# Kernel tuning notes

Hardware: AMD Instinct MI355X
Metric: run time of the kernel (lower is better)

The kernel has to match this reference:

```python
import jax, jax.numpy as jnp
import numpy as np

EPS = 0.01       # perturbation radius (constructor arg)
MEAN = 0.1307    # MNIST normalize constants from the 'else' branch
SIGMA = 0.3081


def _get_bound(v, eps):
    # torch get_bound detaches eps before taking |.| and summing
    r = jnp.sum(jnp.abs(jax.lax.stop_gradient(eps)), axis=-1)
    return v + r, v - r


def _relu_zono(v, eps):
    # v: [N], eps: [N, E]. Append one fresh (zero) error column, as the torch code does.
    n = v.shape[0]
    eps = jnp.concatenate([eps, jnp.zeros((n, 1), eps.dtype)], axis=-1)  # [N, E+1]
    u, l = _get_bound(v, eps)
    denom = u - l  # = 2*sum|eps| >= 0; guard against 0 for non-crossing rows
    # slopes are created as Parameters = u/(u-l) on the first pass (detached leaf)
    slope = jax.lax.stop_gradient(u / jnp.where(denom == 0, 1.0, denom))
    # at init slope == base = u/(u-l), so the slope <= base branch is taken
    term = (1.0 - slope) * u * 0.5
    crossing = (u > 0) & (l < 0)
    dead = u <= 0
    # torch uses slope.data * values.data for the linear part, + term (term carries grad)
    v_cross = jax.lax.stop_gradient(slope * v) + term
    v_new = jnp.where(dead, 0.0, jnp.where(crossing, v_cross, v))
    eps_cross = jnp.concatenate([slope[:, None] * eps[:, :-1], term[:, None]], axis=-1)
    eps_new = jnp.where(dead[:, None], 0.0, jnp.where(crossing[:, None], eps_cross, eps))
    return v_new, eps_new


def _forward(inputs, W1, b1, W2, b2, W3, b3):
    # initial zonotope build (faithful to source: values = u + l, radii = values - l = u)
    upper = jnp.minimum(inputs + EPS, 1.0)   # upper - relu(upper - 1)
    lower = jnp.maximum(inputs - EPS, 0.0)   # relu(lower)
    values = upper + lower
    eps = jnp.diag((values - lower).flatten())  # [D, D]
    # Normalize layer (the 'else' branch)
    values = (values - MEAN) / SIGMA
    eps = eps / SIGMA
    # Flatten
    v = values.flatten()
    # Linear -> ReLU -> Linear -> ReLU -> Linear
    v = W1 @ v + b1
    eps = W1 @ eps
    v, eps = _relu_zono(v, eps)
    v = W2 @ v + b2
    eps = W2 @ eps
    v, eps = _relu_zono(v, eps)
    v = W3 @ v + b3
    eps = W3 @ eps
    u, l = _get_bound(v, eps)
    return u, l


def setup_inputs() -> dict:
    key = jax.random.key(0)
    ks = jax.random.split(key, 7)
    D, H, O = 1024, 4096, 10
    inputs = jax.random.uniform(ks[0], (1, 1, 32, 32), jnp.float32)
    W1 = jax.random.normal(ks[1], (H, D), jnp.float32) / np.float32(np.sqrt(D))
    b1 = jax.random.normal(ks[2], (H,), jnp.float32) * 0.01
    W2 = jax.random.normal(ks[3], (H, H), jnp.float32) / np.float32(np.sqrt(H))
    b2 = jax.random.normal(ks[4], (H,), jnp.float32) * 0.01
    W3 = jax.random.normal(ks[5], (O, H), jnp.float32) / np.float32(np.sqrt(H))
    b3 = jax.random.normal(ks[6], (O,), jnp.float32) * 0.01
    return {"inputs": inputs, "W1": W1, "b1": b1, "W2": W2, "b2": b2, "W3": W3, "b3": b3}


def reference(inputs, W1, b1, W2, b2, W3, b3):
    return _forward(inputs, W1, b1, W2, b2, W3, b3)
```

## Files before the change

kernel.cpp:

```cpp
#include <hip/hip_runtime.h>
#include <math.h>

#define ZEPS  0.01f
#define ZMEAN 0.1307f
#define ZSIGMA 0.3081f

constexpr int D = 1024, H = 4096, O = 10;

using short8 = __attribute__((ext_vector_type(8))) short;
using f32x4  = __attribute__((ext_vector_type(4))) float;
typedef unsigned short ushort_t;

__device__ inline unsigned short f2bf(float x) {
    unsigned int u = __float_as_uint(x);
    u += 0x7FFFu + ((u >> 16) & 1u);
    return (unsigned short)(u >> 16);
}
__device__ inline float bf2f(unsigned short h) {
    return __uint_as_float(((unsigned int)h) << 16);
}

__device__ inline unsigned int f2bf2_fast(float a, float b) {
    unsigned int ua = __float_as_uint(a) + 0x8000u;
    unsigned int ub = __float_as_uint(b) + 0x8000u;
    return (ua >> 16) | (ub & 0xFFFF0000u);
}

__device__ inline void gl_lds16(const void* g, void* l) {
    __builtin_amdgcn_global_load_lds(
        (const __attribute__((address_space(1))) unsigned int*)g,
        (__attribute__((address_space(3))) unsigned int*)l, 16, 0, 0);
}

__device__ inline float zval(float xv) {
    float up = fminf(xv + ZEPS, 1.f);
    float lo = fmaxf(xv - ZEPS, 0.f);
    return (up + lo - ZMEAN) / ZSIGMA;
}
__device__ inline float zdia(float xv) {
    return fminf(xv + ZEPS, 1.f) / ZSIGMA;
}

__device__ inline void relu_params(float v, float r, float& vout, float& aout, float& tout) {
    float u = v + r, l = v - r;
    float denom = u - l;
    float slope = u / (denom == 0.f ? 1.f : denom);
    float term = (1.f - slope) * u * 0.5f;
    bool dead = (u <= 0.f);
    bool crossing = (u > 0.f) && (l < 0.f);
    vout = dead ? 0.f : (crossing ? (slope * v + term) : v);
    aout = dead ? 0.f : (crossing ? slope : 1.f);
    tout = (!dead && crossing) ? term : 0.f;
}

__global__ __launch_bounds__(256) void k_layer1(const float* __restrict__ W1, const float* __restrict__ b1,
                                                const float* __restrict__ x,
                                                float* __restrict__ v1p, float* __restrict__ a1,
                                                float* __restrict__ t1) {
    int wid = threadIdx.x >> 6, lane = threadIdx.x & 63;
    int i = blockIdx.x * 4 + wid;
    const float* row = W1 + (size_t)i * D;
    float sv = 0.f, sr = 0.f;
#pragma unroll
    for (int it = 0; it < 4; ++it) {
        int j = it * 256 + lane * 4;
        float4 w = *(const float4*)&row[j];
        float4 xx = *(const float4*)&x[j];
        sv += w.x * zval(xx.x) + w.y * zval(xx.y) + w.z * zval(xx.z) + w.w * zval(xx.w);
        sr += fabsf(w.x) * zdia(xx.x) + fabsf(w.y) * zdia(xx.y) +
              fabsf(w.z) * zdia(xx.z) + fabsf(w.w) * zdia(xx.w);
    }
#pragma unroll
    for (int m = 1; m <= 32; m <<= 1) {
        sv += __shfl_xor(sv, m, 64);
        sr += __shfl_xor(sr, m, 64);
    }
    if (lane == 0) {
        float vo, ao, to;
        relu_params(sv + b1[i], sr, vo, ao, to);
        v1p[i] = vo; a1[i] = ao; t1[i] = to;
    }
}

__global__ __launch_bounds__(256) void k_scaleT(const float* __restrict__ W1, const float* __restrict__ a1,
                                                const float* __restrict__ x,
                                                ushort_t* __restrict__ W1sT) {
    __shared__ float tile[32][33];
    int j0 = blockIdx.x * 32, k0 = blockIdx.y * 32;
    int r = threadIdx.x >> 3;
    int c = (threadIdx.x & 7) * 4;
    float4 w = *(const float4*)&W1[(size_t)(k0 + r) * D + j0 + c];
    float4 xx = *(const float4*)&x[j0 + c];
    float a = a1[k0 + r];
    tile[r][c + 0] = a * w.x * zdia(xx.x);
    tile[r][c + 1] = a * w.y * zdia(xx.y);
    tile[r][c + 2] = a * w.z * zdia(xx.z);
    tile[r][c + 3] = a * w.w * zdia(xx.w);
    __syncthreads();
    ushort4 o;
    o.x = f2bf(tile[c + 0][r]);
    o.y = f2bf(tile[c + 1][r]);
    o.z = f2bf(tile[c + 2][r]);
    o.w = f2bf(tile[c + 3][r]);
    *(ushort4*)&W1sT[(size_t)(j0 + r) * H + k0 + c] = o;
}

#define GBK 64
__global__ __launch_bounds__(256) void k_gemm_mfma(const float* __restrict__ A,
                                                   const ushort_t* __restrict__ B,
                                                   const float* __restrict__ v1p,
                                                   const float* __restrict__ t1,
                                                   ushort_t* __restrict__ C,
                                                   float* __restrict__ vpart,
                                                   float* __restrict__ tpart) {
    const int N = D, K = H;
    __shared__ __align__(16) ushort_t As[2][128 * GBK];
    __shared__ __align__(16) ushort_t Bs[2][128 * GBK];
    __shared__ float vt[2048], tt[2048];
    int b = blockIdx.x;
    int u = b & 7, v = b >> 3;
    int z = u >> 2;
    int y = (u & 3) * 8 + (v >> 3);
    int xb = v & 7;
    int tid = threadIdx.x;
    int wave = tid >> 6, lane = tid & 63;
    int bm = y * 128, bn = xb * 128;
    int kbeg = z * (K / 2);
    ushort_t* Cz = C + (size_t)z * ((size_t)H * D);
    int wm = (wave >> 1) * 64, wn = (wave & 1) * 64;

    int srow = lane >> 3, sc = lane & 7, scp = sc ^ srow;
    int r15 = lane & 15, quad = lane >> 4, key = r15 & 7;
    int rowg = tid >> 3, ch = tid & 7;
    int aswz = ch ^ (rowg & 7);

    const int S = (K / 2) / GBK;

    float4 pa[4][2];
    float sv[4] = {0.f, 0.f, 0.f, 0.f}, st[4] = {0.f, 0.f, 0.f, 0.f};

    auto issueA = [&](int s) {
#pragma unroll
        for (int g = 0; g < 4; ++g) {
            const float* ap = &A[(size_t)(bm + g * 32 + rowg) * K + kbeg + s * GBK + ch * 8];
            pa[g][0] = *(const float4*)ap;
            pa[g][1] = *(const float4*)(ap + 4);
        }
    };
    auto issueB = [&](int s, int buf) {
#pragma unroll
        for (int g = 0; g < 2; ++g) {
            int row = wave * 32 + g * 16;
            (void)row;
        }
#pragma unroll
        for (int g = 0; g < 4; ++g) {
            int row = wave * 32 + g * 8;
            gl_lds16(&B[(size_t)(bn + row + srow) * K + kbeg + s * GBK + scp * 8], &Bs[buf][row * GBK]);
        }
    };
    auto cvtwrite = [&](int s, int buf) {
        if ((s & 7) == xb) {
            const float* vp = &vt[s * 64 + ch * 8];
            const float* tp = &tt[s * 64 + ch * 8];
            float4 v0 = *(const float4*)vp, v1 = *(const float4*)(vp + 4);
            float4 t0 = *(const float4*)tp, t1v = *(const float4*)(tp + 4);
#pragma unroll
            for (int g = 0; g < 4; ++g) {
                sv[g] += pa[g][0].x * v0.x + pa[g][0].y * v0.y + pa[g][0].z * v0.z + pa[g][0].w * v0.w
                       + pa[g][1].x * v1.x + pa[g][1].y * v1.y + pa[g][1].z * v1.z + pa[g][1].w * v1.w;
                st[g] += pa[g][0].x * t0.x + pa[g][0].y * t0.y + pa[g][0].z * t0.z + pa[g][0].w * t0.w
                       + pa[g][1].x * t1v.x + pa[g][1].y * t1v.y + pa[g][1].z * t1v.z + pa[g][1].w * t1v.w;
            }
        }
#pragma unroll
        for (int g = 0; g < 4; ++g) {
            uint4 hh;
            hh.x = f2bf2_fast(pa[g][0].x, pa[g][0].y);
            hh.y = f2bf2_fast(pa[g][0].z, pa[g][0].w);
            hh.z = f2bf2_fast(pa[g][1].x, pa[g][1].y);
            hh.w = f2bf2_fast(pa[g][1].z, pa[g][1].w);
            *(uint4*)&As[buf][(g * 32 + rowg) * GBK + aswz * 8] = hh;
        }
    };

    f32x4 acc[4][4];
#pragma unroll
    for (int p = 0; p < 4; ++p)
#pragma unroll
        for (int q = 0; q < 4; ++q) acc[p][q] = (f32x4){0.f, 0.f, 0.f, 0.f};

    issueA(0);
    issueB(0, 0);
    for (int idx = tid; idx < 512; idx += 256) {
        *(float4*)&vt[idx * 4] = *(const float4*)&v1p[kbeg + idx * 4];
        *(float4*)&tt[idx * 4] = *(const float4*)&t1[kbeg + idx * 4];
    }
    __syncthreads();
    cvtwrite(0, 0);
    __syncthreads();

    for (int s = 0; s < S; ++s) {
        int buf = s & 1, nbuf = buf ^ 1;
        if (s + 1 < S) {
            issueA(s + 1);
            issueB(s + 1, nbuf);
        }
#pragma unroll
        for (int kk = 0; kk < 2; ++kk) {
            short8 af[4], bf[4];
#pragma unroll
            for (int mt = 0; mt < 4; ++mt)
                af[mt] = *(const short8*)&As[buf][(wm + mt * 16 + r15) * GBK + (((kk * 4 + quad) ^ key)) * 8];
#pragma unroll
            for (int nt = 0; nt < 4; ++nt)
                bf[nt] = *(const short8*)&Bs[buf][(wn + nt * 16 + r15) * GBK + (((kk * 4 + quad) ^ key)) * 8];
#pragma unroll
            for (int mt = 0; mt < 4; ++mt)
#pragma unroll
                for (int nt = 0; nt < 4; ++nt)
                    acc[mt][nt] = __builtin_amdgcn_mfma_f32_16x16x32_bf16(af[mt], bf[nt], acc[mt][nt], 0, 0, 0);
        }
        if (s + 1 < S) cvtwrite(s + 1, nbuf);
        __syncthreads();
    }

#pragma unroll
    for (int mt = 0; mt < 4; ++mt) {
        int gr = bm + wm + mt * 16 + quad * 4;
#pragma unroll
        for (int nt = 0; nt < 4; ++nt) {
            int gc = bn + wn + nt * 16 + r15;
            Cz[(size_t)(gr + 0) * N + gc] = f2bf(acc[mt][nt][0]);
            Cz[(size_t)(gr + 1) * N + gc] = f2bf(acc[mt][nt][1]);
            Cz[(size_t)(gr + 2) * N + gc] = f2bf(acc[mt][nt][2]);
            Cz[(size_t)(gr + 3) * N + gc] = f2bf(acc[mt][nt][3]);
        }
    }

#pragma unroll
    for (int g = 0; g < 4; ++g) {
        float a = sv[g], bb = st[g];
        a += __shfl_xor(a, 1, 64); a += __shfl_xor(a, 2, 64); a += __shfl_xor(a, 4, 64);
        bb += __shfl_xor(bb, 1, 64); bb += __shfl_xor(bb, 2, 64); bb += __shfl_xor(bb, 4, 64);
        if (ch == 0) {
            int i = bm + g * 32 + rowg;
            vpart[(size_t)(z * 8 + xb) * H + i] = a;
            tpart[(size_t)(z * 8 + xb) * H + i] = bb;
        }
    }
}

__global__ __launch_bounds__(256) void k_relu2(const ushort_t* __restrict__ e1, const ushort_t* __restrict__ e2,
                                               const float* __restrict__ vpart, const float* __restrict__ tpart,
                                               const float* __restrict__ b2, const float* __restrict__ W3,
                                               float* __restrict__ v2p, float* __restrict__ a2,
                                               float* __restrict__ t2, float* __restrict__ t2col,
                                               float* __restrict__ w3s) {
    int wid = threadIdx.x >> 6, lane = threadIdx.x & 63;
    int i = blockIdx.x * 4 + wid;
    float s = 0.f;
#pragma unroll
    for (int it = 0; it < 2; ++it) {
        int j = lane * 8 + it * 512;
        ushort4 a0 = *(const ushort4*)&e1[(size_t)i * D + j];
        ushort4 a1v = *(const ushort4*)&e1[(size_t)i * D + j + 4];
        ushort4 b0 = *(const ushort4*)&e2[(size_t)i * D + j];
        ushort4 b1v = *(const ushort4*)&e2[(size_t)i * D + j + 4];
        s += fabsf(bf2f(a0.x) + bf2f(b0.x)) + fabsf(bf2f(a0.y) + bf2f(b0.y))
           + fabsf(bf2f(a0.z) + bf2f(b0.z)) + fabsf(bf2f(a0.w) + bf2f(b0.w))
           + fabsf(bf2f(a1v.x) + bf2f(b1v.x)) + fabsf(bf2f(a1v.y) + bf2f(b1v.y))
           + fabsf(bf2f(a1v.z) + bf2f(b1v.z)) + fabsf(bf2f(a1v.w) + bf2f(b1v.w));
    }
    float ve = (lane < 16) ? vpart[(size_t)lane * H + i] : 0.f;
    float te = (lane < 16) ? tpart[(size_t)lane * H + i] : 0.f;
#pragma unroll
    for (int m = 1; m <= 32; m <<= 1) {
        s += __shfl_xor(s, m, 64);
        ve += __shfl_xor(ve, m, 64);
        te += __shfl_xor(te, m, 64);
    }
    float vo, ao, to;
    relu_params(ve + b2[i], s + fabsf(te), vo, ao, to);
    if (lane == 0) { v2p[i] = vo; a2[i] = ao; t2[i] = to; t2col[i] = te; }
    if (lane < O) w3s[(size_t)i * O + lane] = W3[(size_t)lane * H + i] * ao;
}

__global__ __launch_bounds__(256) void k_eps3a(const ushort_t* __restrict__ e1, const ushort_t* __restrict__ e2,
                                               const float* __restrict__ w3s,
                                               float* __restrict__ pbuf) {
    int jb = blockIdx.x, ib = blockIdx.y;
    int jj = threadIdx.x & 15, s = threadIdx.x >> 4;
    int j = jb * 64 + jj * 4;
    int i0 = ib * 128 + s * 8;
    float acc[4][O];
#pragma unroll
    for (int c = 0; c < 4; ++c)
#pragma unroll
        for (int o = 0; o < O; ++o) acc[c][o] = 0.f;
    for (int ii = 0; ii < 8; ++ii) {
        int i = i0 + ii;
        ushort4 a = *(const ushort4*)&e1[(size_t)i * D + j];
        ushort4 b = *(const ushort4*)&e2[(size_t)i * D + j];
        float e0 = bf2f(a.x) + bf2f(b.x), ee1 = bf2f(a.y) + bf2f(b.y);
        float ee2 = bf2f(a.z) + bf2f(b.z), ee3 = bf2f(a.w) + bf2f(b.w);
        const float* w = &w3s[(size_t)i * O];
#pragma unroll
        for (int o = 0; o < O; ++o) {
            float wo = w[o];
            acc[0][o] += wo * e0; acc[1][o] += wo * ee1;
            acc[2][o] += wo * ee2; acc[3][o] += wo * ee3;
        }
    }
    __shared__ float sm[16][64][O];
#pragma unroll
    for (int c = 0; c < 4; ++c)
#pragma unroll
        for (int o = 0; o < O; ++o) sm[s][jj * 4 + c][o] = acc[c][o];
    __syncthreads();
    for (int idx = threadIdx.x; idx < 64 * O; idx += 256) {
        int col = idx / O, o = idx % O;
        float t = 0.f;
#pragma unroll
        for (int ss = 0; ss < 16; ++ss) t += sm[ss][col][o];
        pbuf[((size_t)o * 32 + ib) * D + jb * 64 + col] = t;
    }
}

__global__ __launch_bounds__(256) void k_final(const float* __restrict__ W3, const float* __restrict__ b3,
                                               const float* __restrict__ v2p, const float* __restrict__ a2,
                                               const float* __restrict__ t2col, const float* __restrict__ t2,
                                               const float* __restrict__ pbuf, float* __restrict__ out) {
    int o = blockIdx.x, tid = threadIdx.x;
    float s3 = 0.f;
    for (int j = tid; j < D; j += 256) {
        float t = 0.f;
#pragma unroll
        for (int ib = 0; ib < 32; ++ib) t += pbuf[((size_t)o * 32 + ib) * D + j];
        s3 += fabsf(t);
    }
    const float* row = W3 + (size_t)o * H;
    float sv = 0.f, s1 = 0.f, s2 = 0.f;
    for (int i = tid; i < H; i += 256) {
        float w = row[i];
        sv += w * v2p[i];
        s1 += w * a2[i] * t2col[i];
        s2 += w * t2[i];
    }
    __shared__ float ra[256], rb[256], rc[256], rd[256];
    ra[tid] = sv; rb[tid] = s1; rc[tid] = s2; rd[tid] = s3;
    __syncthreads();
    for (int off = 128; off; off >>= 1) {
        if (tid < off) {
            ra[tid] += ra[tid + off]; rb[tid] += rb[tid + off];
            rc[tid] += rc[tid + off]; rd[tid] += rd[tid + off];
        }
        __syncthreads();
    }
    if (tid == 0) {
        float v3 = ra[0] + b3[o];
        float rr = rd[0] + fabsf(rb[0]) + fabsf(rc[0]);
        out[o] = v3 + rr;
        out[O + o] = v3 - rr;
    }
}

extern "C" void kernel_launch(void* const* d_in, const int* in_sizes, int n_in,
                              void* d_out, int out_size, void* d_ws, size_t ws_size,
                              hipStream_t stream) {
    const float* x  = (const float*)d_in[0];
    const float* W1 = (const float*)d_in[1];
    const float* b1 = (const float*)d_in[2];
    const float* W2 = (const float*)d_in[3];
    const float* b2 = (const float*)d_in[4];
    const float* W3 = (const float*)d_in[5];
    const float* b3 = (const float*)d_in[6];
    float* out = (float*)d_out;

    float* p = (float*)d_ws;
    float* v1p    = p; p += H;
    float* a1     = p; p += H;
    float* t1     = p; p += H;
    float* t2col  = p; p += H;
    float* v2p    = p; p += H;
    float* a2     = p; p += H;
    float* t2     = p; p += H;
    float* w3s    = p; p += H * O + 8;
    float* vpart  = p; p += 16 * H;
    float* tpart  = p; p += 16 * H;
    float* pbuf   = p; p += 32 * O * D;
    ushort_t* eps2  = (ushort_t*)p;
    ushort_t* W1sT  = eps2 + (size_t)2 * H * D;
    ushort_t* eps2b = eps2 + (size_t)H * D;

    k_layer1<<<H / 4, 256, 0, stream>>>(W1, b1, x, v1p, a1, t1);
    k_scaleT<<<dim3(D / 32, H / 32), 256, 0, stream>>>(W1, a1, x, W1sT);
    k_gemm_mfma<<<512, 256, 0, stream>>>(W2, W1sT, v1p, t1, eps2, vpart, tpart);
    k_relu2<<<H / 4, 256, 0, stream>>>(eps2, eps2b, vpart, tpart, b2, W3, v2p, a2, t2, t2col, w3s);
    k_eps3a<<<dim3(D / 64, 32), 256, 0, stream>>>(eps2, eps2b, w3s, pbuf);
    k_final<<<O, 256, 0, stream>>>(W3, b3, v2p, a2, t2col, t2, pbuf, out);
}
```

Baseline: 201.9 us.

## Split W2 bf16 conversion and matvecs into separate kernel before MFMA GEMM

Adds a kernel that reads W2 in fp32 once, writes a bf16 copy, and computes the W2·v1 and W2·t1 matvecs with a per-row wave reduction. The GEMM then loads both operands as bf16 straight into LDS with global_load_lds, dropping the register-staged fp32 loads, in-loop conversion and partial-sum side work. The block-to-tile mapping changes, and relu2 reads final sums instead of reducing 16 partials. The cost is an extra launch plus a 32 MB bf16 write and re-read of W2, where before each W2 tile was read as fp32 directly inside the GEMM.

```diff
diff --git a/kernel.cpp b/kernel.cpp
--- a/kernel.cpp
+++ b/kernel.cpp
@@ -18,12 +18,6 @@
 }
 __device__ inline float bf2f(unsigned short h) {
     return __uint_as_float(((unsigned int)h) << 16);
-}
-
-__device__ inline unsigned int f2bf2_fast(float a, float b) {
-    unsigned int ua = __float_as_uint(a) + 0x8000u;
-    unsigned int ub = __float_as_uint(b) + 0x8000u;
-    return (ua >> 16) | (ub & 0xFFFF0000u);
 }
 
 __device__ inline void gl_lds16(const void* g, void* l) {
@@ -105,23 +99,49 @@
     *(ushort4*)&W1sT[(size_t)(j0 + r) * H + k0 + c] = o;
 }
 
+__global__ __launch_bounds__(256) void k_w2conv(const float* __restrict__ W2,
+                                                const float* __restrict__ v1p,
+                                                const float* __restrict__ t1,
+                                                ushort_t* __restrict__ W2bf,
+                                                float* __restrict__ v2raw,
+                                                float* __restrict__ t2raw) {
+    int wid = threadIdx.x >> 6, lane = threadIdx.x & 63;
+    int i = blockIdx.x * 4 + wid;
+    const float* row = W2 + (size_t)i * H;
+    ushort_t* orow = W2bf + (size_t)i * H;
+    float sv = 0.f, st = 0.f;
+#pragma unroll 4
+    for (int it = 0; it < 16; ++it) {
+        int j = it * 256 + lane * 4;
+        float4 w = *(const float4*)&row[j];
+        float4 vv = *(const float4*)&v1p[j];
+        float4 tt = *(const float4*)&t1[j];
+        sv += w.x * vv.x + w.y * vv.y + w.z * vv.z + w.w * vv.w;
+        st += w.x * tt.x + w.y * tt.y + w.z * tt.z + w.w * tt.w;
+        ushort4 o;
+        o.x = f2bf(w.x); o.y = f2bf(w.y); o.z = f2bf(w.z); o.w = f2bf(w.w);
+        *(ushort4*)&orow[j] = o;
+    }
+#pragma unroll
+    for (int m = 1; m <= 32; m <<= 1) {
+        sv += __shfl_xor(sv, m, 64);
+        st += __shfl_xor(st, m, 64);
+    }
+    if (lane == 0) { v2raw[i] = sv; t2raw[i] = st; }
+}
+
 #define GBK 64
-__global__ __launch_bounds__(256) void k_gemm_mfma(const float* __restrict__ A,
+__global__ __launch_bounds__(256) void k_gemm_mfma(const ushort_t* __restrict__ A,
                                                    const ushort_t* __restrict__ B,
-                                                   const float* __restrict__ v1p,
-                                                   const float* __restrict__ t1,
-                                                   ushort_t* __restrict__ C,
-                                                   float* __restrict__ vpart,
-                                                   float* __restrict__ tpart) {
+                                                   ushort_t* __restrict__ C) {
     const int N = D, K = H;
     __shared__ __align__(16) ushort_t As[2][128 * GBK];
     __shared__ __align__(16) ushort_t Bs[2][128 * GBK];
-    __shared__ float vt[2048], tt[2048];
     int b = blockIdx.x;
-    int u = b & 7, v = b >> 3;
-    int z = u >> 2;
-    int y = (u & 3) * 8 + (v >> 3);
-    int xb = v & 7;
+    int xb = b & 7;
+    int v = b >> 3;
+    int z = v & 1;
+    int y = v >> 1;
     int tid = threadIdx.x;
     int wave = tid >> 6, lane = tid & 63;
     int bm = y * 128, bn = xb * 128;
@@ -131,58 +151,19 @@
 
     int srow = lane >> 3, sc = lane & 7, scp = sc ^ srow;
     int r15 = lane & 15, quad = lane >> 4, key = r15 & 7;
-    int rowg = tid >> 3, ch = tid & 7;
-    int aswz = ch ^ (rowg & 7);
 
     const int S = (K / 2) / GBK;
 
-    float4 pa[4][2];
-    float sv[4] = {0.f, 0.f, 0.f, 0.f}, st[4] = {0.f, 0.f, 0.f, 0.f};
-
-    auto issueA = [&](int s) {
-#pragma unroll
-        for (int g = 0; g < 4; ++g) {
-            const float* ap = &A[(size_t)(bm + g * 32 + rowg) * K + kbeg + s * GBK + ch * 8];
-            pa[g][0] = *(const float4*)ap;
-            pa[g][1] = *(const float4*)(ap + 4);
-        }
-    };
-    auto issueB = [&](int s, int buf) {
-#pragma unroll
-        for (int g = 0; g < 2; ++g) {
-            int row = wave * 32 + g * 16;
-            (void)row;
-        }
+    auto issue = [&](int s, int buf) {
 #pragma unroll
         for (int g = 0; g < 4; ++g) {
             int row = wave * 32 + g * 8;
-            gl_lds16(&B[(size_t)(bn + row + srow) * K + kbeg + s * GBK + scp * 8], &Bs[buf][row * GBK]);
+            gl_lds16(&A[(size_t)(bm + row + srow) * K + kbeg + s * GBK + scp * 8],
+                     &As[buf][row * GBK]);
+            gl_lds16(&B[(size_t)(bn + row + srow) * K + kbeg + s * GBK + scp * 8],
+                     &Bs[buf][row * GBK]);
         }
     };
-    auto cvtwrite = [&](int s, int buf) {
-        if ((s & 7) == xb) {
-            const float* vp = &vt[s * 64 + ch * 8];
-            const float* tp = &tt[s * 64 + ch * 8];
-            float4 v0 = *(const float4*)vp, v1 = *(const float4*)(vp + 4);
-            float4 t0 = *(const float4*)tp, t1v = *(const float4*)(tp + 4);
-#pragma unroll
-            for (int g = 0; g < 4; ++g) {
-                sv[g] += pa[g][0].x * v0.x + pa[g][0].y * v0.y + pa[g][0].z * v0.z + pa[g][0].w * v0.w
-                       + pa[g][1].x * v1.x + pa[g][1].y * v1.y + pa[g][1].z * v1.z + pa[g][1].w * v1.w;
-                st[g] += pa[g][0].x * t0.x + pa[g][0].y * t0.y + pa[g][0].z * t0.z + pa[g][0].w * t0.w
-                       + pa[g][1].x * t1v.x + pa[g][1].y * t1v.y + pa[g][1].z * t1v.z + pa[g][1].w * t1v.w;
-            }
-        }
-#pragma unroll
-        for (int g = 0; g < 4; ++g) {
-            uint4 hh;
-            hh.x = f2bf2_fast(pa[g][0].x, pa[g][0].y);
-            hh.y = f2bf2_fast(pa[g][0].z, pa[g][0].w);
-            hh.z = f2bf2_fast(pa[g][1].x, pa[g][1].y);
-            hh.w = f2bf2_fast(pa[g][1].z, pa[g][1].w);
-            *(uint4*)&As[buf][(g * 32 + rowg) * GBK + aswz * 8] = hh;
-        }
-    };
 
     f32x4 acc[4][4];
 #pragma unroll
@@ -190,38 +171,27 @@
 #pragma unroll
         for (int q = 0; q < 4; ++q) acc[p][q] = (f32x4){0.f, 0.f, 0.f, 0.f};
 
-    issueA(0);
-    issueB(0, 0);
-    for (int idx = tid; idx < 512; idx += 256) {
-        *(float4*)&vt[idx * 4] = *(const float4*)&v1p[kbeg + idx * 4];
-        *(float4*)&tt[idx * 4] = *(const float4*)&t1[kbeg + idx * 4];
-    }
-    __syncthreads();
-    cvtwrite(0, 0);
+    issue(0, 0);
     __syncthreads();
 
     for (int s = 0; s < S; ++s) {
         int buf = s & 1, nbuf = buf ^ 1;
-        if (s + 1 < S) {
-            issueA(s + 1);
-            issueB(s + 1, nbuf);
-        }
+        if (s + 1 < S) issue(s + 1, nbuf);
 #pragma unroll
         for (int kk = 0; kk < 2; ++kk) {
-            short8 af[4], bf[4];
+            short8 af[4], bfr[4];
 #pragma unroll
             for (int mt = 0; mt < 4; ++mt)
                 af[mt] = *(const short8*)&As[buf][(wm + mt * 16 + r15) * GBK + (((kk * 4 + quad) ^ key)) * 8];
 #pragma unroll
             for (int nt = 0; nt < 4; ++nt)
-                bf[nt] = *(const short8*)&Bs[buf][(wn + nt * 16 + r15) * GBK + (((kk * 4 + quad) ^ key)) * 8];
+                bfr[nt] = *(const short8*)&Bs[buf][(wn + nt * 16 + r15) * GBK + (((kk * 4 + quad) ^ key)) * 8];
 #pragma unroll
             for (int mt = 0; mt < 4; ++mt)
 #pragma unroll
                 for (int nt = 0; nt < 4; ++nt)
-                    acc[mt][nt] = __builtin_amdgcn_mfma_f32_16x16x32_bf16(af[mt], bf[nt], acc[mt][nt], 0, 0, 0);
-        }
-        if (s + 1 < S) cvtwrite(s + 1, nbuf);
+                    acc[mt][nt] = __builtin_amdgcn_mfma_f32_16x16x32_bf16(af[mt], bfr[nt], acc[mt][nt], 0, 0, 0);
+        }
         __syncthreads();
     }
 
@@ -237,22 +207,10 @@
             Cz[(size_t)(gr + 3) * N + gc] = f2bf(acc[mt][nt][3]);
         }
     }
-
-#pragma unroll
-    for (int g = 0; g < 4; ++g) {
-        float a = sv[g], bb = st[g];
-        a += __shfl_xor(a, 1, 64); a += __shfl_xor(a, 2, 64); a += __shfl_xor(a, 4, 64);
-        bb += __shfl_xor(bb, 1, 64); bb += __shfl_xor(bb, 2, 64); bb += __shfl_xor(bb, 4, 64);
-        if (ch == 0) {
-            int i = bm + g * 32 + rowg;
-            vpart[(size_t)(z * 8 + xb) * H + i] = a;
-            tpart[(size_t)(z * 8 + xb) * H + i] = bb;
-        }
-    }
 }
 
 __global__ __launch_bounds__(256) void k_relu2(const ushort_t* __restrict__ e1, const ushort_t* __restrict__ e2,
-                                               const float* __restrict__ vpart, const float* __restrict__ tpart,
+                                               const float* __restrict__ v2raw, const float* __restrict__ t2raw,
                                                const float* __restrict__ b2, const float* __restrict__ W3,
                                                float* __restrict__ v2p, float* __restrict__ a2,
                                                float* __restrict__ t2, float* __restrict__ t2col,
@@ -272,14 +230,10 @@
            + fabsf(bf2f(a1v.x) + bf2f(b1v.x)) + fabsf(bf2f(a1v.y) + bf2f(b1v.y))
            + fabsf(bf2f(a1v.z) + bf2f(b1v.z)) + fabsf(bf2f(a1v.w) + bf2f(b1v.w));
     }
-    float ve = (lane < 16) ? vpart[(size_t)lane * H + i] : 0.f;
-    float te = (lane < 16) ? tpart[(size_t)lane * H + i] : 0.f;
-#pragma unroll
-    for (int m = 1; m <= 32; m <<= 1) {
-        s += __shfl_xor(s, m, 64);
-        ve += __shfl_xor(ve, m, 64);
-        te += __shfl_xor(te, m, 64);
-    }
+#pragma unroll
+    for (int m = 1; m <= 32; m <<= 1) s += __shfl_xor(s, m, 64);
+    float ve = v2raw[i];
+    float te = t2raw[i];
     float vo, ao, to;
     relu_params(ve + b2[i], s + fabsf(te), vo, ao, to);
     if (lane == 0) { v2p[i] = vo; a2[i] = ao; t2[i] = to; t2col[i] = te; }
@@ -385,18 +339,20 @@
     float* v2p    = p; p += H;
     float* a2     = p; p += H;
     float* t2     = p; p += H;
+    float* v2raw  = p; p += H;
+    float* t2raw  = p; p += H;
     float* w3s    = p; p += H * O + 8;
-    float* vpart  = p; p += 16 * H;
-    float* tpart  = p; p += 16 * H;
     float* pbuf   = p; p += 32 * O * D;
     ushort_t* eps2  = (ushort_t*)p;
     ushort_t* W1sT  = eps2 + (size_t)2 * H * D;
+    ushort_t* W2bf  = W1sT + (size_t)H * D;
     ushort_t* eps2b = eps2 + (size_t)H * D;
 
     k_layer1<<<H / 4, 256, 0, stream>>>(W1, b1, x, v1p, a1, t1);
     k_scaleT<<<dim3(D / 32, H / 32), 256, 0, stream>>>(W1, a1, x, W1sT);
-    k_gemm_mfma<<<512, 256, 0, stream>>>(W2, W1sT, v1p, t1, eps2, vpart, tpart);
-    k_relu2<<<H / 4, 256, 0, stream>>>(eps2, eps2b, vpart, tpart, b2, W3, v2p, a2, t2, t2col, w3s);
+    k_w2conv<<<H / 4, 256, 0, stream>>>(W2, v1p, t1, W2bf, v2raw, t2raw);
+    k_gemm_mfma<<<512, 256, 0, stream>>>(W2bf, W1sT, eps2);
+    k_relu2<<<H / 4, 256, 0, stream>>>(eps2, eps2b, v2raw, t2raw, b2, W3, v2p, a2, t2, t2col, w3s);
     k_eps3a<<<dim3(D / 64, 32), 256, 0, stream>>>(eps2, eps2b, w3s, pbuf);
     k_final<<<O, 256, 0, stream>>>(W3, b3, v2p, a2, t2col, t2, pbuf, out);
 }
```

Result: slower. 215.7 us (+6.9%).

## Fuse second ReLU and eps3 reduction into one kernel with atomic partials

Applied to the files above, without the earlier changes.

Merges k_relu2 and k_eps3a into a single kernel. Each block computes ReLU parameters for 16 rows, keeps the scaled W3 slice in shared memory, then reads the same bf16 eps rows again to accumulate the W3 product. The per-block partials are atomically added into 32 interleaved buffers, which are zeroed by extra blocks added to k_layer1. This removes one launch, the w3s global round trip and the shared-memory reduction. In exchange it adds atomic contention, and with 256 blocks there is less parallelism than the old 1024-block and 512-block grids.

```diff
diff --git a/kernel.cpp b/kernel.cpp
--- a/kernel.cpp
+++ b/kernel.cpp
@@ -8,6 +8,7 @@
 constexpr int D = 1024, H = 4096, O = 10;
 
 using short8 = __attribute__((ext_vector_type(8))) short;
+using us8    = __attribute__((ext_vector_type(8))) unsigned short;
 using f32x4  = __attribute__((ext_vector_type(4))) float;
 typedef unsigned short ushort_t;
 
@@ -56,9 +57,15 @@
 __global__ __launch_bounds__(256) void k_layer1(const float* __restrict__ W1, const float* __restrict__ b1,
                                                 const float* __restrict__ x,
                                                 float* __restrict__ v1p, float* __restrict__ a1,
-                                                float* __restrict__ t1) {
+                                                float* __restrict__ t1, float* __restrict__ pbufP) {
+    int b = blockIdx.x;
+    if (b >= 1024) {
+        size_t base = (size_t)(b - 1024) * 5120;
+        for (int k = threadIdx.x; k < 5120; k += 256) pbufP[base + k] = 0.f;
+        return;
+    }
     int wid = threadIdx.x >> 6, lane = threadIdx.x & 63;
-    int i = blockIdx.x * 4 + wid;
+    int i = b * 4 + wid;
     const float* row = W1 + (size_t)i * D;
     float sv = 0.f, sr = 0.f;
 #pragma unroll
@@ -149,11 +156,6 @@
     };
     auto issueB = [&](int s, int buf) {
 #pragma unroll
-        for (int g = 0; g < 2; ++g) {
-            int row = wave * 32 + g * 16;
-            (void)row;
-        }
-#pragma unroll
         for (int g = 0; g < 4; ++g) {
             int row = wave * 32 + g * 8;
             gl_lds16(&B[(size_t)(bn + row + srow) * K + kbeg + s * GBK + scp * 8], &Bs[buf][row * GBK]);
@@ -251,92 +253,85 @@
     }
 }
 
-__global__ __launch_bounds__(256) void k_relu2(const ushort_t* __restrict__ e1, const ushort_t* __restrict__ e2,
-                                               const float* __restrict__ vpart, const float* __restrict__ tpart,
-                                               const float* __restrict__ b2, const float* __restrict__ W3,
-                                               float* __restrict__ v2p, float* __restrict__ a2,
-                                               float* __restrict__ t2, float* __restrict__ t2col,
-                                               float* __restrict__ w3s) {
-    int wid = threadIdx.x >> 6, lane = threadIdx.x & 63;
-    int i = blockIdx.x * 4 + wid;
-    float s = 0.f;
-#pragma unroll
-    for (int it = 0; it < 2; ++it) {
-        int j = lane * 8 + it * 512;
-        ushort4 a0 = *(const ushort4*)&e1[(size_t)i * D + j];
-        ushort4 a1v = *(const ushort4*)&e1[(size_t)i * D + j + 4];
-        ushort4 b0 = *(const ushort4*)&e2[(size_t)i * D + j];
-        ushort4 b1v = *(const ushort4*)&e2[(size_t)i * D + j + 4];
-        s += fabsf(bf2f(a0.x) + bf2f(b0.x)) + fabsf(bf2f(a0.y) + bf2f(b0.y))
-           + fabsf(bf2f(a0.z) + bf2f(b0.z)) + fabsf(bf2f(a0.w) + bf2f(b0.w))
-           + fabsf(bf2f(a1v.x) + bf2f(b1v.x)) + fabsf(bf2f(a1v.y) + bf2f(b1v.y))
-           + fabsf(bf2f(a1v.z) + bf2f(b1v.z)) + fabsf(bf2f(a1v.w) + bf2f(b1v.w));
-    }
-    float ve = (lane < 16) ? vpart[(size_t)lane * H + i] : 0.f;
-    float te = (lane < 16) ? tpart[(size_t)lane * H + i] : 0.f;
-#pragma unroll
-    for (int m = 1; m <= 32; m <<= 1) {
-        s += __shfl_xor(s, m, 64);
-        ve += __shfl_xor(ve, m, 64);
-        te += __shfl_xor(te, m, 64);
-    }
-    float vo, ao, to;
-    relu_params(ve + b2[i], s + fabsf(te), vo, ao, to);
-    if (lane == 0) { v2p[i] = vo; a2[i] = ao; t2[i] = to; t2col[i] = te; }
-    if (lane < O) w3s[(size_t)i * O + lane] = W3[(size_t)lane * H + i] * ao;
-}
-
-__global__ __launch_bounds__(256) void k_eps3a(const ushort_t* __restrict__ e1, const ushort_t* __restrict__ e2,
-                                               const float* __restrict__ w3s,
-                                               float* __restrict__ pbuf) {
-    int jb = blockIdx.x, ib = blockIdx.y;
-    int jj = threadIdx.x & 15, s = threadIdx.x >> 4;
-    int j = jb * 64 + jj * 4;
-    int i0 = ib * 128 + s * 8;
+__global__ __launch_bounds__(256) void k_epsfuse(const ushort_t* __restrict__ e1, const ushort_t* __restrict__ e2,
+                                                 const float* __restrict__ vpart, const float* __restrict__ tpart,
+                                                 const float* __restrict__ b2, const float* __restrict__ W3,
+                                                 float* __restrict__ v2p, float* __restrict__ a2,
+                                                 float* __restrict__ t2, float* __restrict__ t2col,
+                                                 float* __restrict__ pbufP) {
+    __shared__ float w3sm[16][O];
+    int b = blockIdx.x, tid = threadIdx.x;
+    int wid = tid >> 6, lane = tid & 63;
+    int i0 = b * 16;
+
+#pragma unroll
+    for (int rr = 0; rr < 4; ++rr) {
+        int il = wid * 4 + rr;
+        int i = i0 + il;
+        const ushort_t* p1 = &e1[(size_t)i * D + lane * 16];
+        const ushort_t* p2 = &e2[(size_t)i * D + lane * 16];
+        float s = 0.f;
+#pragma unroll
+        for (int q = 0; q < 2; ++q) {
+            us8 u1 = *(const us8*)(p1 + q * 8);
+            us8 u2 = *(const us8*)(p2 + q * 8);
+#pragma unroll
+            for (int e = 0; e < 8; ++e) s += fabsf(bf2f(u1[e]) + bf2f(u2[e]));
+        }
+        float ve = (lane < 16) ? vpart[(size_t)lane * H + i] : 0.f;
+        float te = (lane < 16) ? tpart[(size_t)lane * H + i] : 0.f;
+#pragma unroll
+        for (int m = 1; m <= 32; m <<= 1) {
+            s += __shfl_xor(s, m, 64);
+            ve += __shfl_xor(ve, m, 64);
+            te += __shfl_xor(te, m, 64);
+        }
+        float vo, ao, to;
+        relu_params(ve + b2[i], s + fabsf(te), vo, ao, to);
+        if (lane == 0) { v2p[i] = vo; a2[i] = ao; t2[i] = to; t2col[i] = te; }
+        if (lane < O) w3sm[il][lane] = W3[(size_t)lane * H + i] * ao;
+    }
+    __syncthreads();
+
+    int j = tid * 4;
     float acc[4][O];
 #pragma unroll
     for (int c = 0; c < 4; ++c)
 #pragma unroll
         for (int o = 0; o < O; ++o) acc[c][o] = 0.f;
-    for (int ii = 0; ii < 8; ++ii) {
-        int i = i0 + ii;
+#pragma unroll 4
+    for (int il = 0; il < 16; ++il) {
+        int i = i0 + il;
         ushort4 a = *(const ushort4*)&e1[(size_t)i * D + j];
-        ushort4 b = *(const ushort4*)&e2[(size_t)i * D + j];
-        float e0 = bf2f(a.x) + bf2f(b.x), ee1 = bf2f(a.y) + bf2f(b.y);
-        float ee2 = bf2f(a.z) + bf2f(b.z), ee3 = bf2f(a.w) + bf2f(b.w);
-        const float* w = &w3s[(size_t)i * O];
+        ushort4 bb = *(const ushort4*)&e2[(size_t)i * D + j];
+        float es0 = bf2f(a.x) + bf2f(bb.x), es1 = bf2f(a.y) + bf2f(bb.y);
+        float es2 = bf2f(a.z) + bf2f(bb.z), es3 = bf2f(a.w) + bf2f(bb.w);
+        const float* w = &w3sm[il][0];
 #pragma unroll
         for (int o = 0; o < O; ++o) {
             float wo = w[o];
-            acc[0][o] += wo * e0; acc[1][o] += wo * ee1;
-            acc[2][o] += wo * ee2; acc[3][o] += wo * ee3;
-        }
-    }
-    __shared__ float sm[16][64][O];
-#pragma unroll
-    for (int c = 0; c < 4; ++c)
-#pragma unroll
-        for (int o = 0; o < O; ++o) sm[s][jj * 4 + c][o] = acc[c][o];
-    __syncthreads();
-    for (int idx = threadIdx.x; idx < 64 * O; idx += 256) {
-        int col = idx / O, o = idx % O;
-        float t = 0.f;
-#pragma unroll
-        for (int ss = 0; ss < 16; ++ss) t += sm[ss][col][o];
-        pbuf[((size_t)o * 32 + ib) * D + jb * 64 + col] = t;
-    }
+            acc[0][o] += wo * es0; acc[1][o] += wo * es1;
+            acc[2][o] += wo * es2; acc[3][o] += wo * es3;
+        }
+    }
+    float* pg = &pbufP[(size_t)(b & 31) * O * D];
+#pragma unroll
+    for (int o = 0; o < O; ++o)
+#pragma unroll
+        for (int c = 0; c < 4; ++c)
+            atomicAdd(&pg[(size_t)o * D + j + c], acc[c][o]);
 }
 
 __global__ __launch_bounds__(256) void k_final(const float* __restrict__ W3, const float* __restrict__ b3,
                                                const float* __restrict__ v2p, const float* __restrict__ a2,
                                                const float* __restrict__ t2col, const float* __restrict__ t2,
-                                               const float* __restrict__ pbuf, float* __restrict__ out) {
+                                               const float* __restrict__ pbufP, float* __restrict__ out) {
     int o = blockIdx.x, tid = threadIdx.x;
     float s3 = 0.f;
     for (int j = tid; j < D; j += 256) {
         float t = 0.f;
 #pragma unroll
-        for (int ib = 0; ib < 32; ++ib) t += pbuf[((size_t)o * 32 + ib) * D + j];
+        for (int g = 0; g < 32; ++g) t += pbufP[((size_t)g * O + o) * D + j];
         s3 += fabsf(t);
     }
     const float* row = W3 + (size_t)o * H;
@@ -385,18 +380,16 @@
     float* v2p    = p; p += H;
     float* a2     = p; p += H;
     float* t2     = p; p += H;
-    float* w3s    = p; p += H * O + 8;
     float* vpart  = p; p += 16 * H;
     float* tpart  = p; p += 16 * H;
-    float* pbuf   = p; p += 32 * O * D;
+    float* pbufP  = p; p += 32 * O * D + 8;
     ushort_t* eps2  = (ushort_t*)p;
     ushort_t* W1sT  = eps2 + (size_t)2 * H * D;
     ushort_t* eps2b = eps2 + (size_t)H * D;
 
-    k_layer1<<<H / 4, 256, 0, stream>>>(W1, b1, x, v1p, a1, t1);
+    k_layer1<<<1088, 256, 0, stream>>>(W1, b1, x, v1p, a1, t1, pbufP);
     k_scaleT<<<dim3(D / 32, H / 32), 256, 0, stream>>>(W1, a1, x, W1sT);
     k_gemm_mfma<<<512, 256, 0, stream>>>(W2, W1sT, v1p, t1, eps2, vpart, tpart);
-    k_relu2<<<H / 4, 256, 0, stream>>>(eps2, eps2b, vpart, tpart, b2, W3, v2p, a2, t2, t2col, w3s);
-    k_eps3a<<<dim3(D / 64, 32), 256, 0, stream>>>(eps2, eps2b, w3s, pbuf);
-    k_final<<<O, 256, 0, stream>>>(W3, b3, v2p, a2, t2col, t2, pbuf, out);
-}
+    k_epsfuse<<<256, 256, 0, stream>>>(eps2, eps2b, vpart, tpart, b2, W3, v2p, a2, t2, t2col, pbufP);
+    k_final<<<O, 256, 0, stream>>>(W3, b3, v2p, a2, t2col, t2, pbufP, out);
+}
```

After: 235.5 us. 1.17x slower.
